# Performance work log

Hardware: AMD Instinct MI355X
Metric: run time of the kernel (lower is better)

Reference implementation:

```python
import jax, jax.numpy as jnp
import numpy as np

N = 100000   # nodes
E = 1600000  # edges
F = 64       # input_features == output_features
BN_EPS = 1e-5


def _bn(x, gamma, beta):
    # torch BatchNorm1d (training mode): biased batch statistics
    mu = jnp.mean(x, axis=0)
    var = jnp.var(x, axis=0)
    return (x - mu) * jax.lax.rsqrt(var + BN_EPS) * gamma + beta


def setup_inputs() -> dict:
    key = jax.random.key(0)
    ks = jax.random.split(key, 16)
    s = 0.05
    inp = {
        'node_feats': jax.random.normal(ks[0], (N, F), jnp.float32),
        'edge_feats': jax.random.normal(ks[1], (E, F), jnp.float32),
        'src': jax.random.randint(ks[2], (E,), 0, N, jnp.int32),
        'dst': jax.random.randint(ks[3], (E,), 0, N, jnp.int32),
        # linear params: W [F_in, F_out], b [F_out]
        'W_src_gate': jax.random.normal(ks[4], (F, F), jnp.float32) * s,
        'b_src_gate': jnp.zeros((F,), jnp.float32),
        'W_dst_gate': jax.random.normal(ks[5], (F, F), jnp.float32) * s,
        'b_dst_gate': jnp.zeros((F,), jnp.float32),
        'W_edge_gate': jax.random.normal(ks[6], (F, F), jnp.float32) * s,
        'b_edge_gate': jnp.zeros((F,), jnp.float32),
        'W_src_update': jax.random.normal(ks[7], (F, F), jnp.float32) * s,
        'b_src_update': jnp.zeros((F,), jnp.float32),
        'W_dst_update': jax.random.normal(ks[8], (F, F), jnp.float32) * s,
        'b_dst_update': jnp.zeros((F,), jnp.float32),
        'bn_nodes_gamma': jnp.ones((F,), jnp.float32),
        'bn_nodes_beta': jnp.zeros((F,), jnp.float32),
        'bn_edges_gamma': jnp.ones((F,), jnp.float32),
        'bn_edges_beta': jnp.zeros((F,), jnp.float32),
    }
    return inp


def reference(node_feats, edge_feats, src, dst,
              W_src_gate, b_src_gate, W_dst_gate, b_dst_gate,
              W_edge_gate, b_edge_gate, W_src_update, b_src_update,
              W_dst_update, b_dst_update,
              bn_nodes_gamma, bn_nodes_beta, bn_edges_gamma, bn_edges_beta):
    # EdgeGatedGraphConv (arXiv:1711.07553), residual=True
    e_src = node_feats @ W_src_gate + b_src_gate          # [N,F]
    e_dst = node_feats @ W_dst_gate + b_dst_gate          # [N,F]
    # u_add_v gather + edge transform -> gate logits m [E,F]
    m = e_src[src] + e_dst[dst] + (edge_feats @ W_edge_gate + b_edge_gate)
    sigma = jax.nn.sigmoid(m)                             # [E,F]
    Bh = node_feats @ W_dst_update + b_dst_update         # [N,F]
    # u_mul_e message + scatter-sum to destination nodes
    sum_sigma_h = jax.ops.segment_sum(Bh[src] * sigma, dst, num_segments=node_feats.shape[0])
    sum_sigma = jax.ops.segment_sum(sigma, dst, num_segments=node_feats.shape[0])
    h = sum_sigma_h / (sum_sigma + 1e-6)                  # normalized aggregation
    x = node_feats @ W_src_update + b_src_update + h
    x = jax.nn.silu(_bn(x, bn_nodes_gamma, bn_nodes_beta))
    y = jax.nn.silu(_bn(m, bn_edges_gamma, bn_edges_beta))
    x = node_feats + x   # residual
    y = edge_feats + y   # residual
    return (x, y)
```

## Files before the change

kernel.cpp:

```cpp
#include <hip/hip_runtime.h>
#include <hip/hip_bf16.h>

typedef __attribute__((ext_vector_type(8))) __bf16 bf16x8;
typedef __attribute__((ext_vector_type(4))) float f32x4;

#define MFMA(a,b,c) __builtin_amdgcn_mfma_f32_16x16x32_bf16((a),(b),(c),0,0,0)

__device__ __forceinline__ bf16x8 cvt8(float4 a, float4 b){
  bf16x8 r;
  r[0]=(__bf16)a.x; r[1]=(__bf16)a.y; r[2]=(__bf16)a.z; r[3]=(__bf16)a.w;
  r[4]=(__bf16)b.x; r[5]=(__bf16)b.y; r[6]=(__bf16)b.z; r[7]=(__bf16)b.w;
  return r;
}

__global__ void setup_k(const float* __restrict__ W_sg, const float* __restrict__ W_dg,
                        const float* __restrict__ W_eg, const float* __restrict__ W_su,
                        const float* __restrict__ W_du,
                        bf16x8* __restrict__ Wp, bf16x8* __restrict__ Wq,
                        int4* __restrict__ zp, int nz4){
  if (blockIdx.x < 16){
    int tid = blockIdx.x*256 + threadIdx.x;
    if (tid >= 2560 + 1536) return;
    int lane = tid & 63, g = lane>>4, c = lane&15;
    if (tid < 2560){
      int frag = (tid>>6)&7, m = tid>>9;
      const float* Ws[5] = {W_sg, W_dg, W_eg, W_su, W_du};
      const float* W = Ws[m];
      int kt = frag>>2, nt = frag&3;
      bf16x8 v;
      #pragma unroll
      for (int j=0;j<8;j++) v[j] = (__bf16)W[(kt*32+g*8+j)*64 + nt*16 + c];
      Wp[tid] = v;
    } else {
      int t2 = tid - 2560;
      int frag = (t2>>6)&7, m = t2>>9;
      const float* Ws[3] = {W_eg, W_sg, W_dg};
      const float* W = Ws[m];
      int mt = frag>>1, kh = frag&1;
      bf16x8 v;
      #pragma unroll
      for (int j=0;j<8;j++) v[j] = (__bf16)W[(kh*32+g*8+j)*64 + mt*16 + c];
      Wq[t2] = v;
    }
  } else {
    int i = (blockIdx.x-16)*256 + threadIdx.x, st = (gridDim.x-16)*256;
    for (; i<nz4; i+=st) zp[i] = make_int4(0,0,0,0);
  }
}

__global__ __launch_bounds__(256) void xform_hist_k(
    const float* __restrict__ nf, const bf16x8* __restrict__ Wp,
    const float* __restrict__ b_su, const float* __restrict__ b_du,
    float* __restrict__ A_src, float* __restrict__ Bh, int ntiles, int nxf,
    const int* __restrict__ dst, int* __restrict__ cnt, int E)
{
  if ((int)blockIdx.x < nxf){
    int lane = threadIdx.x & 63;
    int gw = blockIdx.x*4 + (threadIdx.x>>6);
    if (gw >= ntiles) return;
    int g = lane>>4, c = lane&15;
    long base = (long)gw*16;
    const float* rp = nf + (base + c)*64 + g*8;
    float4 a0 = *(const float4*)rp,      a1 = *(const float4*)(rp+4);
    float4 a2 = *(const float4*)(rp+32), a3 = *(const float4*)(rp+36);
    bf16x8 A0 = cvt8(a0,a1), A1 = cvt8(a2,a3);
    const float* biases[2] = {b_su,b_du};
    float* outs[2] = {A_src,Bh};
    const int mats[2] = {3,4};
    #pragma unroll
    for (int i=0;i<2;i++){
      #pragma unroll
      for (int nt=0;nt<4;nt++){
        f32x4 acc = {0.f,0.f,0.f,0.f};
        acc = MFMA(A0, Wp[(mats[i]*8+nt)*64+lane],   acc);
        acc = MFMA(A1, Wp[(mats[i]*8+4+nt)*64+lane], acc);
        int col = c + nt*16;
        float bb = biases[i][col];
        #pragma unroll
        for (int e=0;e<4;e++) outs[i][(base+4*g+e)*64 + col] = acc[e] + bb;
      }
    }
  } else {
    int nb = gridDim.x - nxf;
    int i = (blockIdx.x-nxf)*256 + threadIdx.x, st = nb*256;
    for (; i<E; i+=st) atomicAdd(&cnt[dst[i]], 1);
  }
}

__global__ __launch_bounds__(1024) void scan_k(const int* __restrict__ cnt,
                                               int* __restrict__ row, int Nn){
  __shared__ int part[1024];
  int t = threadIdx.x;
  int C = (Nn + 1023) >> 10;
  int lo = t*C;
  int hi = lo + C; if (hi > Nn) hi = Nn;
  int s = 0;
  for (int i=lo; i<hi; i++) s += cnt[i];
  part[t] = s;
  __syncthreads();
  for (int off=1; off<1024; off<<=1){
    int v = part[t];
    int u = (t>=off) ? part[t-off] : 0;
    __syncthreads();
    part[t] = v + u;
    __syncthreads();
  }
  int excl = (t==0) ? 0 : part[t-1];
  for (int i=lo; i<hi; i++){ row[i] = excl; excl += cnt[i]; }
  if (t==1023) row[Nn] = excl;
}

#define NFILL 1024
__global__ __launch_bounds__(256) void fillA_k(
    const int* __restrict__ src, const int* __restrict__ dst,
    const int* __restrict__ rowp, int* __restrict__ cnt2,
    int2* __restrict__ pairs, int E,
    const float* __restrict__ ef, const float* __restrict__ nf,
    const float* __restrict__ b_sg, const float* __restrict__ b_dg,
    const float* __restrict__ b_eg,
    const bf16x8* __restrict__ Wq,
    __bf16* __restrict__ m16, int ntiles)
{
  __shared__ bf16x8 wl[24*64];
  if (blockIdx.x < NFILL){
    int i = blockIdx.x*256 + threadIdx.x, st = NFILL*256;
    for (; i<E; i+=st){
      int d = dst[i];
      int pos = rowp[d] + atomicAdd(&cnt2[d], 1);
      pairs[pos] = make_int2(i, src[i]);
    }
    return;
  }
  {
    int t = threadIdx.x;
    #pragma unroll
    for (int i=0;i<6;i++) wl[i*256+t] = Wq[i*256+t];
  }
  __syncthreads();
  int lane = threadIdx.x & 63, g = lane>>4, c = lane&15;
  int gw = (blockIdx.x-NFILL)*4 + (threadIdx.x>>6);
  int nw = (gridDim.x-NFILL)*4;
  float bias2[4][4];
  #pragma unroll
  for (int mt=0;mt<4;mt++)
    #pragma unroll
    for (int e=0;e<4;e++){
      int f = mt*16 + 4*g + e;
      bias2[mt][e] = b_sg[f] + b_dg[f] + b_eg[f];
    }
  int sc = 0, dc = 0;
  if (gw < ntiles){ sc = src[(long)gw*16 + c]; dc = dst[(long)gw*16 + c]; }
  for (int tt=gw; tt<ntiles; tt+=nw){
    long base = (long)tt*16;
    int tn = tt + nw;
    int sn = sc, dn = dc;
    if (tn < ntiles){ sn = src[(long)tn*16 + c]; dn = dst[(long)tn*16 + c]; }
    const float* rpe = ef + (base+c)*64 + g*8;
    const float* rps = nf + (long)sc*64 + g*8;
    const float* rpd = nf + (long)dc*64 + g*8;
    float4 e0=*(const float4*)rpe,      e1=*(const float4*)(rpe+4);
    float4 e2=*(const float4*)(rpe+32), e3=*(const float4*)(rpe+36);
    float4 s0=*(const float4*)rps,      s1=*(const float4*)(rps+4);
    float4 s2=*(const float4*)(rps+32), s3=*(const float4*)(rps+36);
    float4 d0=*(const float4*)rpd,      d1=*(const float4*)(rpd+4);
    float4 d2=*(const float4*)(rpd+32), d3=*(const float4*)(rpd+36);
    bf16x8 BE0=cvt8(e0,e1), BE1=cvt8(e2,e3);
    bf16x8 BS0=cvt8(s0,s1), BS1=cvt8(s2,s3);
    bf16x8 BD0=cvt8(d0,d1), BD1=cvt8(d2,d3);
    #pragma unroll
    for (int mt=0;mt<4;mt++){
      f32x4 am = {0.f,0.f,0.f,0.f};
      am = MFMA(wl[((0*4+mt)*2+0)*64+lane], BE0, am);
      am = MFMA(wl[((0*4+mt)*2+1)*64+lane], BE1, am);
      am = MFMA(wl[((1*4+mt)*2+0)*64+lane], BS0, am);
      am = MFMA(wl[((1*4+mt)*2+1)*64+lane], BS1, am);
      am = MFMA(wl[((2*4+mt)*2+0)*64+lane], BD0, am);
      am = MFMA(wl[((2*4+mt)*2+1)*64+lane], BD1, am);
      union { __bf16 h[4]; uint2 u; } pk;
      #pragma unroll
      for (int e=0;e<4;e++) pk.h[e] = (__bf16)(am[e] + bias2[mt][e]);
      *(uint2*)(m16 + (base+c)*64 + mt*16 + 4*g) = pk.u;
    }
    sc = sn; dc = dn;
  }
}

__global__ __launch_bounds__(256) void phaseB(
    const __bf16* __restrict__ m16, const int2* __restrict__ pairs,
    const float* __restrict__ Bh, const int* __restrict__ rowp,
    float* __restrict__ A_src,
    float* __restrict__ est, float* __restrict__ nst, int Nn)
{
  __shared__ float sst[256];
  sst[threadIdx.x] = 0.f;
  __syncthreads();
  int lane = threadIdx.x & 63, w = threadIdx.x>>6;
  int chunk = (Nn + gridDim.x - 1)/gridDim.x;
  int n0 = blockIdx.x*chunk;
  int n1 = n0 + chunk; if (n1 > Nn) n1 = Nn;
  float e1=0.f, e2=0.f, p1=0.f, p2=0.f;
  for (int n=n0+w; n<n1; n+=4){
    int r0 = rowp[n], r1 = rowp[n+1];
    float ssum=0.f, bsum=0.f;
    int r = r0;
    for (; r+8 <= r1; r+=8){
      int2 q[8];
      #pragma unroll
      for (int j=0;j<8;j++) q[j] = pairs[r+j];
      float mv[8], bh[8];
      #pragma unroll
      for (int j=0;j<8;j++) mv[j] = (float)m16[(long)q[j].x*64 + lane];
      #pragma unroll
      for (int j=0;j<8;j++) bh[j] = Bh[(long)q[j].y*64 + lane];
      #pragma unroll
      for (int j=0;j<8;j++){
        float sg = 1.f/(1.f+__expf(-mv[j]));
        ssum += sg; bsum += bh[j]*sg;
        e1 += mv[j]; e2 += mv[j]*mv[j];
      }
    }
    for (; r < r1; ++r){
      int2 q0 = pairs[r];
      float mv0 = (float)m16[(long)q0.x*64 + lane];
      float bh0 = Bh[(long)q0.y*64 + lane];
      float sg0 = 1.f/(1.f+__expf(-mv0));
      ssum += sg0; bsum += bh0*sg0;
      e1 += mv0;   e2 += mv0*mv0;
    }
    long xi = (long)n*64 + lane;
    float xp = A_src[xi] + bsum/(ssum+1e-6f);
    A_src[xi] = xp;
    p1 += xp; p2 += xp*xp;
  }
  atomicAdd(&sst[lane],     e1);
  atomicAdd(&sst[64+lane],  e2);
  atomicAdd(&sst[128+lane], p1);
  atomicAdd(&sst[192+lane], p2);
  __syncthreads();
  int t = threadIdx.x;
  if (t < 128) atomicAdd(&est[t], sst[t]);
  else         atomicAdd(&nst[t-128], sst[t]);
}

#define NNF 1024
__global__ __launch_bounds__(256) void finals_k(
    const float* __restrict__ nf, const float* __restrict__ xpre,
    const float* __restrict__ nst, const float* __restrict__ gn,
    const float* __restrict__ btn, float* __restrict__ xo, int Nn,
    const __bf16* __restrict__ m16, const float* __restrict__ ef,
    const float* __restrict__ est, const float* __restrict__ ge,
    const float* __restrict__ bte, float* __restrict__ y, float invE, long E)
{
  if (blockIdx.x < NNF){
    long tid = (long)blockIdx.x*256 + threadIdx.x;
    long stride = (long)NNF*256;
    int col = (int)(tid & 63);
    float invN = 1.f/(float)Nn;
    float mu = nst[col]*invN;
    float var = nst[64+col]*invN - mu*mu;
    float rs = rsqrtf(var + 1e-5f);
    float aa = gn[col]*rs;
    float bb = btn[col] - mu*aa;
    long total = (long)Nn*64;
    for (long i=tid; i<total; i+=stride){
      float z = xpre[i]*aa + bb;
      xo[i] = nf[i] + z/(1.f+__expf(-z));
    }
  } else {
    int oct = threadIdx.x & 7;
    float aa[8], bb[8];
    #pragma unroll
    for (int j=0;j<8;j++){
      int col = oct*8 + j;
      float mu = est[col]*invE;
      float var = est[64+col]*invE - mu*mu;
      float rs = rsqrtf(var + 1e-5f);
      float ga = ge[col]*rs;
      aa[j] = ga; bb[j] = bte[col] - mu*ga;
    }
    long tid = (long)(blockIdx.x-NNF)*256 + threadIdx.x;
    long pstep = ((long)(gridDim.x-NNF)*256) >> 3;
    for (long p = tid>>3; p < E; p += pstep){
      bf16x8 mv = *(const bf16x8*)&m16[p*64 + oct*8];
      const float* rp = ef + p*64 + oct*8;
      float4 f0 = *(const float4*)rp, f1 = *(const float4*)(rp+4);
      float o[8];
      #pragma unroll
      for (int j=0;j<8;j++){
        float z = aa[j]*(float)mv[j] + bb[j];
        float ev = (j<4) ? ((const float*)&f0)[j] : ((const float*)&f1)[j-4];
        o[j] = ev + z/(1.f+__expf(-z));
      }
      float* yp = y + p*64 + oct*8;
      *(float4*)yp     = make_float4(o[0],o[1],o[2],o[3]);
      *(float4*)(yp+4) = make_float4(o[4],o[5],o[6],o[7]);
    }
  }
}

extern "C" void kernel_launch(void* const* d_in, const int* in_sizes, int n_in,
                              void* d_out, int out_size, void* d_ws, size_t ws_size,
                              hipStream_t stream){
  const float* nf  = (const float*)d_in[0];
  const float* ef  = (const float*)d_in[1];
  const int*   src = (const int*)d_in[2];
  const int*   dst = (const int*)d_in[3];
  const float* W_sg=(const float*)d_in[4];  const float* b_sg=(const float*)d_in[5];
  const float* W_dg=(const float*)d_in[6];  const float* b_dg=(const float*)d_in[7];
  const float* W_eg=(const float*)d_in[8];  const float* b_eg=(const float*)d_in[9];
  const float* W_su=(const float*)d_in[10]; const float* b_su=(const float*)d_in[11];
  const float* W_du=(const float*)d_in[12]; const float* b_du=(const float*)d_in[13];
  const float* gn=(const float*)d_in[14];   const float* btn=(const float*)d_in[15];
  const float* ge=(const float*)d_in[16];   const float* bte=(const float*)d_in[17];

  int Nn = in_sizes[0]/64;
  int Ee = in_sizes[2];
  size_t Nf = (size_t)Nn*64;
  size_t Es = (size_t)Ee;

  float* ws    = (float*)d_ws;
  float* A_src = ws;
  float* Bh    = ws + Nf;
  __bf16* m16  = (__bf16*)(ws + 2*Nf);
  int2*  pairs = (int2*)(ws + 2*Nf + 32*Es);
  int*   cnt   = (int*)(pairs + Es);
  int*   cnt2  = cnt + Nn;
  float* est   = (float*)(cnt2 + Nn);
  float* nst   = est + 128;
  int*   rowp  = (int*)(nst + 128);
  size_t woff  = 2*Nf + 32*Es + 2*Es + 2*(size_t)Nn + 256 + (size_t)Nn + 1;
  woff = (woff + 15) & ~(size_t)15;
  bf16x8* Wp   = (bf16x8*)(ws + woff);
  bf16x8* Wq   = Wp + 2560;

  float* xo = (float*)d_out;
  float* yo = xo + Nf;

  int nz4 = (int)((2*(size_t)Nn + 256) >> 2);
  setup_k<<<272,256,0,stream>>>(W_sg,W_dg,W_eg,W_su,W_du,Wp,Wq,(int4*)cnt,nz4);

  int ntn = Nn/16;
  int nxf = (ntn+3)/4;
  xform_hist_k<<<nxf+2048,256,0,stream>>>(nf,Wp,b_su,b_du,A_src,Bh,ntn,nxf,
                                          dst,cnt,Ee);
  scan_k<<<1,1024,0,stream>>>(cnt,rowp,Nn);
  int nte = Ee/16;
  fillA_k<<<NFILL+4096,256,0,stream>>>(src,dst,rowp,cnt2,pairs,Ee,
                                       ef,nf,b_sg,b_dg,b_eg,Wq,m16,nte);
  phaseB<<<4096,256,0,stream>>>(m16,pairs,Bh,rowp,A_src,est,nst,Nn);
  finals_k<<<NNF+4096,256,0,stream>>>(nf,A_src,nst,gn,btn,xo,Nn,
                                      m16,ef,est,ge,bte,yo,
                                      1.f/(float)Ee,(long)Ee);
}
```

Baseline: 932.2 us.

## Software-pipeline edge tile loads in fillA and pair-index loads in phaseB

In fillA_k, the gathered edge and node feature rows for the next tile are loaded into registers while the current tile's MFMAs run, and the src/dst indices are prefetched two tiles ahead. In phaseB, the next batch of eight (edge, src) pairs is prefetched before the current batch's m16/Bh gathers are consumed. The aim is to hide global-memory gather latency behind compute. The cost is higher register pressure, which may lower occupancy.

```diff
diff --git a/kernel.cpp b/kernel.cpp
--- a/kernel.cpp
+++ b/kernel.cpp
@@ -110,6 +110,26 @@
   if (t==1023) row[Nn] = excl;
 }
 
+struct TileF {
+  float4 e0,e1,e2,e3,s0,s1,s2,s3,d0,d1,d2,d3;
+};
+
+__device__ __forceinline__ TileF ld_tile(const float* __restrict__ ef,
+                                         const float* __restrict__ nf,
+                                         long base, int c, int g, int sc, int dc){
+  TileF t;
+  const float* rpe = ef + (base+c)*64 + g*8;
+  const float* rps = nf + (long)sc*64 + g*8;
+  const float* rpd = nf + (long)dc*64 + g*8;
+  t.e0=*(const float4*)rpe;      t.e1=*(const float4*)(rpe+4);
+  t.e2=*(const float4*)(rpe+32); t.e3=*(const float4*)(rpe+36);
+  t.s0=*(const float4*)rps;      t.s1=*(const float4*)(rps+4);
+  t.s2=*(const float4*)(rps+32); t.s3=*(const float4*)(rps+36);
+  t.d0=*(const float4*)rpd;      t.d1=*(const float4*)(rpd+4);
+  t.d2=*(const float4*)(rpd+32); t.d3=*(const float4*)(rpd+36);
+  return t;
+}
+
 #define NFILL 1024
 __global__ __launch_bounds__(256) void fillA_k(
     const int* __restrict__ src, const int* __restrict__ dst,
@@ -148,25 +168,22 @@
       int f = mt*16 + 4*g + e;
       bias2[mt][e] = b_sg[f] + b_dg[f] + b_eg[f];
     }
-  int sc = 0, dc = 0;
-  if (gw < ntiles){ sc = src[(long)gw*16 + c]; dc = dst[(long)gw*16 + c]; }
+  if (gw >= ntiles) return;
+  int sc = src[(long)gw*16 + c], dc = dst[(long)gw*16 + c];
+  TileF cur = ld_tile(ef, nf, (long)gw*16, c, g, sc, dc);
+  int t1i = gw + nw;
+  int sn = sc, dn = dc;
+  if (t1i < ntiles){ sn = src[(long)t1i*16 + c]; dn = dst[(long)t1i*16 + c]; }
   for (int tt=gw; tt<ntiles; tt+=nw){
+    int t1 = tt + nw;
+    TileF nxt;
+    if (t1 < ntiles) nxt = ld_tile(ef, nf, (long)t1*16, c, g, sn, dn);
+    int t2 = t1 + nw;
+    if (t2 < ntiles){ sn = src[(long)t2*16 + c]; dn = dst[(long)t2*16 + c]; }
+    bf16x8 BE0=cvt8(cur.e0,cur.e1), BE1=cvt8(cur.e2,cur.e3);
+    bf16x8 BS0=cvt8(cur.s0,cur.s1), BS1=cvt8(cur.s2,cur.s3);
+    bf16x8 BD0=cvt8(cur.d0,cur.d1), BD1=cvt8(cur.d2,cur.d3);
     long base = (long)tt*16;
-    int tn = tt + nw;
-    int sn = sc, dn = dc;
-    if (tn < ntiles){ sn = src[(long)tn*16 + c]; dn = dst[(long)tn*16 + c]; }
-    const float* rpe = ef + (base+c)*64 + g*8;
-    const float* rps = nf + (long)sc*64 + g*8;
-    const float* rpd = nf + (long)dc*64 + g*8;
-    float4 e0=*(const float4*)rpe,      e1=*(const float4*)(rpe+4);
-    float4 e2=*(const float4*)(rpe+32), e3=*(const float4*)(rpe+36);
-    float4 s0=*(const float4*)rps,      s1=*(const float4*)(rps+4);
-    float4 s2=*(const float4*)(rps+32), s3=*(const float4*)(rps+36);
-    float4 d0=*(const float4*)rpd,      d1=*(const float4*)(rpd+4);
-    float4 d2=*(const float4*)(rpd+32), d3=*(const float4*)(rpd+36);
-    bf16x8 BE0=cvt8(e0,e1), BE1=cvt8(e2,e3);
-    bf16x8 BS0=cvt8(s0,s1), BS1=cvt8(s2,s3);
-    bf16x8 BD0=cvt8(d0,d1), BD1=cvt8(d2,d3);
     #pragma unroll
     for (int mt=0;mt<4;mt++){
       f32x4 am = {0.f,0.f,0.f,0.f};
@@ -181,7 +198,7 @@
       for (int e=0;e<4;e++) pk.h[e] = (__bf16)(am[e] + bias2[mt][e]);
       *(uint2*)(m16 + (base+c)*64 + mt*16 + 4*g) = pk.u;
     }
-    sc = sn; dc = dn;
+    cur = nxt;
   }
 }
 
@@ -203,10 +220,20 @@
     int r0 = rowp[n], r1 = rowp[n+1];
     float ssum=0.f, bsum=0.f;
     int r = r0;
-    for (; r+8 <= r1; r+=8){
-      int2 q[8];
+    int2 q[8];
+    bool have = (r + 8 <= r1);
+    if (have){
       #pragma unroll
       for (int j=0;j<8;j++) q[j] = pairs[r+j];
+    }
+    while (have){
+      int rn = r + 8;
+      bool haven = (rn + 8 <= r1);
+      int2 qn[8];
+      if (haven){
+        #pragma unroll
+        for (int j=0;j<8;j++) qn[j] = pairs[rn+j];
+      }
       float mv[8], bh[8];
       #pragma unroll
       for (int j=0;j<8;j++) mv[j] = (float)m16[(long)q[j].x*64 + lane];
@@ -218,6 +245,11 @@
         ssum += sg; bsum += bh[j]*sg;
         e1 += mv[j]; e2 += mv[j]*mv[j];
       }
+      if (haven){
+        #pragma unroll
+        for (int j=0;j<8;j++) q[j] = qn[j];
+      }
+      r = rn; have = haven;
     }
     for (; r < r1; ++r){
       int2 q0 = pairs[r];
```

Result: no change. 933.2 us (+0.1%).

## Precompute per-node gate projections in bf16 instead of per-edge node GEMMs

Applied to the files above, without the earlier changes.

Node-level src/dst gate projections and the update projection are now computed once per node in the transform kernel and stored as bf16. The edge kernel gathers these bf16 rows and adds them through identity-matrix MFMAs, instead of gathering fp32 node features and running two extra 64x64 GEMMs per edge. Bh is also stored as bf16, and biases move into phaseB. This cuts per-edge gather bytes and MFMA work, at the cost of extra bf16 rounding on the gathered projections.

```diff
diff --git a/kernel.cpp b/kernel.cpp
--- a/kernel.cpp
+++ b/kernel.cpp
@@ -16,32 +16,20 @@
 __global__ void setup_k(const float* __restrict__ W_sg, const float* __restrict__ W_dg,
                         const float* __restrict__ W_eg, const float* __restrict__ W_su,
                         const float* __restrict__ W_du,
-                        bf16x8* __restrict__ Wp, bf16x8* __restrict__ Wq,
+                        bf16x8* __restrict__ Wq,
                         int4* __restrict__ zp, int nz4){
   if (blockIdx.x < 16){
     int tid = blockIdx.x*256 + threadIdx.x;
-    if (tid >= 2560 + 1536) return;
+    if (tid >= 2560) return;
     int lane = tid & 63, g = lane>>4, c = lane&15;
-    if (tid < 2560){
-      int frag = (tid>>6)&7, m = tid>>9;
-      const float* Ws[5] = {W_sg, W_dg, W_eg, W_su, W_du};
-      const float* W = Ws[m];
-      int kt = frag>>2, nt = frag&3;
-      bf16x8 v;
-      #pragma unroll
-      for (int j=0;j<8;j++) v[j] = (__bf16)W[(kt*32+g*8+j)*64 + nt*16 + c];
-      Wp[tid] = v;
-    } else {
-      int t2 = tid - 2560;
-      int frag = (t2>>6)&7, m = t2>>9;
-      const float* Ws[3] = {W_eg, W_sg, W_dg};
-      const float* W = Ws[m];
-      int mt = frag>>1, kh = frag&1;
-      bf16x8 v;
-      #pragma unroll
-      for (int j=0;j<8;j++) v[j] = (__bf16)W[(kh*32+g*8+j)*64 + mt*16 + c];
-      Wq[t2] = v;
-    }
+    int frag = (tid>>6)&7, m = tid>>9;
+    const float* Ws[5] = {W_eg, W_sg, W_dg, W_du, W_su};
+    const float* W = Ws[m];
+    int mt = frag>>1, kh = frag&1;
+    bf16x8 v;
+    #pragma unroll
+    for (int j=0;j<8;j++) v[j] = (__bf16)W[(kh*32+g*8+j)*64 + mt*16 + c];
+    Wq[tid] = v;
   } else {
     int i = (blockIdx.x-16)*256 + threadIdx.x, st = (gridDim.x-16)*256;
     for (; i<nz4; i+=st) zp[i] = make_int4(0,0,0,0);
@@ -49,9 +37,9 @@
 }
 
 __global__ __launch_bounds__(256) void xform_hist_k(
-    const float* __restrict__ nf, const bf16x8* __restrict__ Wp,
-    const float* __restrict__ b_su, const float* __restrict__ b_du,
-    float* __restrict__ A_src, float* __restrict__ Bh, int ntiles, int nxf,
+    const float* __restrict__ nf, const bf16x8* __restrict__ Wq,
+    __bf16* __restrict__ es16, __bf16* __restrict__ ed16,
+    __bf16* __restrict__ bh16, float* __restrict__ A_src, int ntiles, int nxf,
     const int* __restrict__ dst, int* __restrict__ cnt, int E)
 {
   if ((int)blockIdx.x < nxf){
@@ -63,22 +51,29 @@
     const float* rp = nf + (base + c)*64 + g*8;
     float4 a0 = *(const float4*)rp,      a1 = *(const float4*)(rp+4);
     float4 a2 = *(const float4*)(rp+32), a3 = *(const float4*)(rp+36);
-    bf16x8 A0 = cvt8(a0,a1), A1 = cvt8(a2,a3);
-    const float* biases[2] = {b_su,b_du};
-    float* outs[2] = {A_src,Bh};
-    const int mats[2] = {3,4};
-    #pragma unroll
-    for (int i=0;i<2;i++){
-      #pragma unroll
-      for (int nt=0;nt<4;nt++){
-        f32x4 acc = {0.f,0.f,0.f,0.f};
-        acc = MFMA(A0, Wp[(mats[i]*8+nt)*64+lane],   acc);
-        acc = MFMA(A1, Wp[(mats[i]*8+4+nt)*64+lane], acc);
-        int col = c + nt*16;
-        float bb = biases[i][col];
+    bf16x8 B0 = cvt8(a0,a1), B1 = cvt8(a2,a3);
+    __bf16* outs[3] = {es16, ed16, bh16};
+    const int mats[3] = {1,2,3};
+    #pragma unroll
+    for (int i=0;i<3;i++){
+      #pragma unroll
+      for (int mt=0;mt<4;mt++){
+        f32x4 am = {0.f,0.f,0.f,0.f};
+        am = MFMA(Wq[(mats[i]*8+mt*2+0)*64+lane], B0, am);
+        am = MFMA(Wq[(mats[i]*8+mt*2+1)*64+lane], B1, am);
+        union { __bf16 h[4]; uint2 u; } pk;
         #pragma unroll
-        for (int e=0;e<4;e++) outs[i][(base+4*g+e)*64 + col] = acc[e] + bb;
+        for (int e=0;e<4;e++) pk.h[e] = (__bf16)am[e];
+        *(uint2*)(outs[i] + (base+c)*64 + mt*16 + 4*g) = pk.u;
       }
+    }
+    #pragma unroll
+    for (int mt=0;mt<4;mt++){
+      f32x4 am = {0.f,0.f,0.f,0.f};
+      am = MFMA(Wq[(4*8+mt*2+0)*64+lane], B0, am);
+      am = MFMA(Wq[(4*8+mt*2+1)*64+lane], B1, am);
+      *(float4*)(A_src + (base+c)*64 + mt*16 + 4*g) =
+        make_float4(am[0],am[1],am[2],am[3]);
     }
   } else {
     int nb = gridDim.x - nxf;
@@ -115,13 +110,14 @@
     const int* __restrict__ src, const int* __restrict__ dst,
     const int* __restrict__ rowp, int* __restrict__ cnt2,
     int2* __restrict__ pairs, int E,
-    const float* __restrict__ ef, const float* __restrict__ nf,
+    const float* __restrict__ ef,
+    const __bf16* __restrict__ es16, const __bf16* __restrict__ ed16,
     const float* __restrict__ b_sg, const float* __restrict__ b_dg,
     const float* __restrict__ b_eg,
     const bf16x8* __restrict__ Wq,
     __bf16* __restrict__ m16, int ntiles)
 {
-  __shared__ bf16x8 wl[24*64];
+  __shared__ bf16x8 wl[8*64];
   if (blockIdx.x < NFILL){
     int i = blockIdx.x*256 + threadIdx.x, st = NFILL*256;
     for (; i<E; i+=st){
@@ -134,10 +130,16 @@
   {
     int t = threadIdx.x;
     #pragma unroll
-    for (int i=0;i<6;i++) wl[i*256+t] = Wq[i*256+t];
+    for (int i=0;i<2;i++) wl[i*256+t] = Wq[i*256+t];
   }
   __syncthreads();
   int lane = threadIdx.x & 63, g = lane>>4, c = lane&15;
+  bf16x8 I0, I1;
+  #pragma unroll
+  for (int j=0;j<8;j++){
+    I0[j] = (g*8+j == c)      ? (__bf16)1.0f : (__bf16)0.0f;
+    I1[j] = (g*8+j == 16 + c) ? (__bf16)1.0f : (__bf16)0.0f;
+  }
   int gw = (blockIdx.x-NFILL)*4 + (threadIdx.x>>6);
   int nw = (gridDim.x-NFILL)*4;
   float bias2[4][4];
@@ -148,34 +150,29 @@
       int f = mt*16 + 4*g + e;
       bias2[mt][e] = b_sg[f] + b_dg[f] + b_eg[f];
     }
-  int sc = 0, dc = 0;
-  if (gw < ntiles){ sc = src[(long)gw*16 + c]; dc = dst[(long)gw*16 + c]; }
+  if (gw >= ntiles) return;
+  int sc = src[(long)gw*16 + c], dc = dst[(long)gw*16 + c];
   for (int tt=gw; tt<ntiles; tt+=nw){
     long base = (long)tt*16;
     int tn = tt + nw;
     int sn = sc, dn = dc;
     if (tn < ntiles){ sn = src[(long)tn*16 + c]; dn = dst[(long)tn*16 + c]; }
     const float* rpe = ef + (base+c)*64 + g*8;
-    const float* rps = nf + (long)sc*64 + g*8;
-    const float* rpd = nf + (long)dc*64 + g*8;
     float4 e0=*(const float4*)rpe,      e1=*(const float4*)(rpe+4);
     float4 e2=*(const float4*)(rpe+32), e3=*(const float4*)(rpe+36);
-    float4 s0=*(const float4*)rps,      s1=*(const float4*)(rps+4);
-    float4 s2=*(const float4*)(rps+32), s3=*(const float4*)(rps+36);
-    float4 d0=*(const float4*)rpd,      d1=*(const float4*)(rpd+4);
-    float4 d2=*(const float4*)(rpd+32), d3=*(const float4*)(rpd+36);
+    bf16x8 BS0 = *(const bf16x8*)(es16 + (long)sc*64 + g*8);
+    bf16x8 BS1 = *(const bf16x8*)(es16 + (long)sc*64 + 32 + g*8);
+    bf16x8 BD0 = *(const bf16x8*)(ed16 + (long)dc*64 + g*8);
+    bf16x8 BD1 = *(const bf16x8*)(ed16 + (long)dc*64 + 32 + g*8);
     bf16x8 BE0=cvt8(e0,e1), BE1=cvt8(e2,e3);
-    bf16x8 BS0=cvt8(s0,s1), BS1=cvt8(s2,s3);
-    bf16x8 BD0=cvt8(d0,d1), BD1=cvt8(d2,d3);
     #pragma unroll
     for (int mt=0;mt<4;mt++){
+      bf16x8 Is = (mt&1) ? I1 : I0;
       f32x4 am = {0.f,0.f,0.f,0.f};
-      am = MFMA(wl[((0*4+mt)*2+0)*64+lane], BE0, am);
-      am = MFMA(wl[((0*4+mt)*2+1)*64+lane], BE1, am);
-      am = MFMA(wl[((1*4+mt)*2+0)*64+lane], BS0, am);
-      am = MFMA(wl[((1*4+mt)*2+1)*64+lane], BS1, am);
-      am = MFMA(wl[((2*4+mt)*2+0)*64+lane], BD0, am);
-      am = MFMA(wl[((2*4+mt)*2+1)*64+lane], BD1, am);
+      am = MFMA(wl[(mt*2+0)*64+lane], BE0, am);
+      am = MFMA(wl[(mt*2+1)*64+lane], BE1, am);
+      am = MFMA(Is, (mt>>1) ? BS1 : BS0, am);
+      am = MFMA(Is, (mt>>1) ? BD1 : BD0, am);
       union { __bf16 h[4]; uint2 u; } pk;
       #pragma unroll
       for (int e=0;e<4;e++) pk.h[e] = (__bf16)(am[e] + bias2[mt][e]);
@@ -187,7 +184,8 @@
 
 __global__ __launch_bounds__(256) void phaseB(
     const __bf16* __restrict__ m16, const int2* __restrict__ pairs,
-    const float* __restrict__ Bh, const int* __restrict__ rowp,
+    const __bf16* __restrict__ bh16, const int* __restrict__ rowp,
+    const float* __restrict__ b_du, const float* __restrict__ b_su,
     float* __restrict__ A_src,
     float* __restrict__ est, float* __restrict__ nst, int Nn)
 {
@@ -195,6 +193,7 @@
   sst[threadIdx.x] = 0.f;
   __syncthreads();
   int lane = threadIdx.x & 63, w = threadIdx.x>>6;
+  float bdu = b_du[lane], bsu = b_su[lane];
   int chunk = (Nn + gridDim.x - 1)/gridDim.x;
   int n0 = blockIdx.x*chunk;
   int n1 = n0 + chunk; if (n1 > Nn) n1 = Nn;
@@ -211,7 +210,7 @@
       #pragma unroll
       for (int j=0;j<8;j++) mv[j] = (float)m16[(long)q[j].x*64 + lane];
       #pragma unroll
-      for (int j=0;j<8;j++) bh[j] = Bh[(long)q[j].y*64 + lane];
+      for (int j=0;j<8;j++) bh[j] = (float)bh16[(long)q[j].y*64 + lane] + bdu;
       #pragma unroll
       for (int j=0;j<8;j++){
         float sg = 1.f/(1.f+__expf(-mv[j]));
@@ -222,13 +221,13 @@
     for (; r < r1; ++r){
       int2 q0 = pairs[r];
       float mv0 = (float)m16[(long)q0.x*64 + lane];
-      float bh0 = Bh[(long)q0.y*64 + lane];
+      float bh0 = (float)bh16[(long)q0.y*64 + lane] + bdu;
       float sg0 = 1.f/(1.f+__expf(-mv0));
       ssum += sg0; bsum += bh0*sg0;
       e1 += mv0;   e2 += mv0*mv0;
     }
     long xi = (long)n*64 + lane;
-    float xp = A_src[xi] + bsum/(ssum+1e-6f);
+    float xp = A_src[xi] + bsu + bsum/(ssum+1e-6f);
     A_src[xi] = xp;
     p1 += xp; p2 += xp*xp;
   }
@@ -320,34 +319,35 @@
 
   float* ws    = (float*)d_ws;
   float* A_src = ws;
-  float* Bh    = ws + Nf;
-  __bf16* m16  = (__bf16*)(ws + 2*Nf);
-  int2*  pairs = (int2*)(ws + 2*Nf + 32*Es);
+  __bf16* es16 = (__bf16*)(ws + Nf);
+  __bf16* ed16 = (__bf16*)(ws + Nf + Nf/2);
+  __bf16* bh16 = (__bf16*)(ws + 2*Nf);
+  __bf16* m16  = (__bf16*)(ws + 2*Nf + Nf/2);
+  int2*  pairs = (int2*)(ws + 2*Nf + Nf/2 + 32*Es);
   int*   cnt   = (int*)(pairs + Es);
   int*   cnt2  = cnt + Nn;
   float* est   = (float*)(cnt2 + Nn);
   float* nst   = est + 128;
   int*   rowp  = (int*)(nst + 128);
-  size_t woff  = 2*Nf + 32*Es + 2*Es + 2*(size_t)Nn + 256 + (size_t)Nn + 1;
+  size_t woff  = 2*Nf + Nf/2 + 32*Es + 2*Es + 2*(size_t)Nn + 256 + (size_t)Nn + 1;
   woff = (woff + 15) & ~(size_t)15;
-  bf16x8* Wp   = (bf16x8*)(ws + woff);
-  bf16x8* Wq   = Wp + 2560;
+  bf16x8* Wq   = (bf16x8*)(ws + woff);
 
   float* xo = (float*)d_out;
   float* yo = xo + Nf;
 
   int nz4 = (int)((2*(size_t)Nn + 256) >> 2);
-  setup_k<<<272,256,0,stream>>>(W_sg,W_dg,W_eg,W_su,W_du,Wp,Wq,(int4*)cnt,nz4);
+  setup_k<<<272,256,0,stream>>>(W_sg,W_dg,W_eg,W_su,W_du,Wq,(int4*)cnt,nz4);
 
   int ntn = Nn/16;
   int nxf = (ntn+3)/4;
-  xform_hist_k<<<nxf+2048,256,0,stream>>>(nf,Wp,b_su,b_du,A_src,Bh,ntn,nxf,
+  xform_hist_k<<<nxf+2048,256,0,stream>>>(nf,Wq,es16,ed16,bh16,A_src,ntn,nxf,
                                           dst,cnt,Ee);
   scan_k<<<1,1024,0,stream>>>(cnt,rowp,Nn);
   int nte = Ee/16;
   fillA_k<<<NFILL+4096,256,0,stream>>>(src,dst,rowp,cnt2,pairs,Ee,
-                                       ef,nf,b_sg,b_dg,b_eg,Wq,m16,nte);
-  phaseB<<<4096,256,0,stream>>>(m16,pairs,Bh,rowp,A_src,est,nst,Nn);
+                                       ef,es16,ed16,b_sg,b_dg,b_eg,Wq,m16,nte);
+  phaseB<<<4096,256,0,stream>>>(m16,pairs,bh16,rowp,b_du,b_su,A_src,est,nst,Nn);
   finals_k<<<NNF+4096,256,0,stream>>>(nf,A_src,nst,gn,btn,xo,Nn,
                                       m16,ef,est,ge,bte,yo,
                                       1.f/(float)Ee,(long)Ee);
```

Result: faster. 902.5 us (-3.2%).
